# Kernel optimization log

Measured on AMD Instinct MI355X. Metric: run time of the kernel, lower is better.

The kernel has to match this reference:

```python
import jax, jax.numpy as jnp
import numpy as np

N_QUBITS, Q_DEPTH, N_OUTPUT, BATCH = 8, 6, 8, 16384
_C = np.complex64
_H = (np.array([[1, 1], [1, -1]]) / np.sqrt(2)).astype(_C)
_PX = np.array([[0, 1], [1, 0]], dtype=_C)
_PY = np.array([[0, -1j], [1j, 0]], dtype=_C)
_PZ = np.array([[1, 0], [0, -1]], dtype=_C)

def _swap_rows(n, i, j):
    m = np.eye(n, dtype=_C)
    m[[i, j]] = m[[j, i]]
    return m

_CNOT = _swap_rows(4, 2, 3)          # flip target when control=1
_CZ = np.diag(np.array([1, 1, 1, -1], dtype=_C))
_CSWAP = _swap_rows(8, 5, 6)         # swap |101> <-> |110>
_TOF = _swap_rows(8, 6, 7)           # swap |110> <-> |111>


def _apply(state, U, wires):
    """Apply k-qubit gate U (2^k x 2^k, shared across batch) on given wires.
    state: [B] + [2]*N_QUBITS complex tensor."""
    k = len(wires)
    axes = [w + 1 for w in wires]
    st = jnp.moveaxis(state, axes, list(range(1, k + 1)))
    shp = st.shape
    st = jnp.einsum('ij,bjr->bir', jnp.asarray(U, st.dtype), st.reshape(shp[0], 2 ** k, -1))
    return jnp.moveaxis(st.reshape(shp), list(range(1, k + 1)), axes)


def _apply_batched(state, U, wire):
    """Apply per-sample single-qubit gate U [B,2,2] on `wire`."""
    st = jnp.moveaxis(state, wire + 1, 1)
    shp = st.shape
    st = jnp.einsum('bij,bjr->bir', U, st.reshape(shp[0], 2, -1))
    return jnp.moveaxis(st.reshape(shp), 1, wire + 1)


def _rot_mat(axis, theta):
    """Scalar-angle RX/RY/RZ (axis 0/1/2), PennyLane convention exp(-i theta P / 2)."""
    c = jnp.cos(theta / 2)
    s = jnp.sin(theta / 2)
    z = jnp.zeros_like(c)
    if axis == 0:    # RX
        re = jnp.stack([jnp.stack([c, z]), jnp.stack([z, c])])
        im = jnp.stack([jnp.stack([z, -s]), jnp.stack([-s, z])])
    elif axis == 1:  # RY
        re = jnp.stack([jnp.stack([c, -s]), jnp.stack([s, c])])
        im = jnp.zeros((2, 2), dtype=c.dtype)
    else:            # RZ
        re = jnp.stack([jnp.stack([c, z]), jnp.stack([z, c])])
        im = jnp.stack([jnp.stack([-s, z]), jnp.stack([z, s])])
    return (re.astype(jnp.complex64) + 1j * im.astype(jnp.complex64))


def _ry_batched(theta):
    """Per-sample RY matrices: theta [B] -> [B,2,2] complex64."""
    c = jnp.cos(theta / 2)
    s = jnp.sin(theta / 2)
    U = jnp.stack([jnp.stack([c, -s], -1), jnp.stack([s, c], -1)], -2)
    return U.astype(jnp.complex64)


def _forward(input_features, q_params, d_ry, d_rot, d_g2):
    B = input_features.shape[0]
    n = N_QUBITS
    qw = q_params.reshape(Q_DEPTH, n)
    # |0...0> state, shape [B] + [2]*n
    basis = jnp.zeros((2 ** n,), jnp.complex64).at[0].set(1.0)
    state = (jnp.ones((B, 1), jnp.complex64) * basis[None, :]).reshape((B,) + (2,) * n)
    for w in range(n):
        state = _apply(state, _H, [w])
    two_q = {5: _CNOT, 8: _CZ}
    three_q = {6: _CSWAP, 7: _TOF}
    one_q = {1: _H, 2: _PX, 3: _PY, 4: _PZ}
    for layer in range(Q_DEPTH):
        for node in range(n):
            li, ni = layer % 6, node % 4
            if d_ry[li, ni]:
                state = _apply_batched(state, _ry_batched(input_features[:, node]), node)
            rot = int(d_rot[li, ni])
            if rot < 3:
                state = _apply(state, _rot_mat(rot, qw[layer, node]), [node])
            g2 = int(d_g2[li, ni])
            if g2 in one_q:
                state = _apply(state, one_q[g2], [node])
            elif g2 in two_q:
                state = _apply(state, two_q[g2], [node, (node + 1) % n])
            elif g2 in three_q:
                state = _apply(state, three_q[g2], [node, (node + 1) % n, (node + 2) % n])
    probs = state.real ** 2 + state.imag ** 2  # [B] + [2]*n
    exps = []
    for p in range(N_OUTPUT):
        axes = tuple(i for i in range(1, n + 1) if i != p + 1)
        m = probs.sum(axis=axes)  # [B, 2]
        exps.append(m[:, 0] - m[:, 1])
    return jnp.stack(exps, axis=1)  # [B, N_OUTPUT] float32


def setup_inputs() -> dict:
    key = jax.random.key(0)
    k1, k2, k3, k4, k5 = jax.random.split(key, 5)
    return {
        'input_features': jax.random.normal(k1, (BATCH, N_QUBITS), jnp.float32),
        'q_params': jax.random.normal(k2, (Q_DEPTH * N_QUBITS,), jnp.float32),
        'design_ry': jax.random.randint(k3, (6, 4), 0, 2, jnp.int32),
        'design_rot': jax.random.randint(k4, (6, 4), 0, 4, jnp.int32),
        'design_gate2': jax.random.randint(k5, (6, 4), 0, 9, jnp.int32),
    }


def reference(input_features, q_params, design_ry, design_rot, design_gate2):
    # The circuit design is a static (architecture) choice -> host constants.
    d_ry = np.asarray(design_ry)
    d_rot = np.asarray(design_rot)
    d_g2 = np.asarray(design_gate2)
    return _forward(input_features, q_params, d_ry, d_rot, d_g2)
```

## Files before the change

kernel.cpp:

```cpp
#include <hip/hip_runtime.h>
#include <stdint.h>

#define NQ 8

#define HALF_INV2PI 0.07957747154594767f

typedef float f32x2 __attribute__((ext_vector_type(2)));

__device__ __forceinline__ f32x2 pk2(float x, float y) { f32x2 r; r.x = x; r.y = y; return r; }
__device__ __forceinline__ f32x2 pkb(float x)          { f32x2 r; r.x = x; r.y = x; return r; }

__device__ __forceinline__ f32x2 pk_fma(f32x2 a, f32x2 b, f32x2 c) {
    f32x2 d;
    asm("v_pk_fma_f32 %0, %1, %2, %3" : "=v"(d) : "v"(a), "v"(b), "v"(c));
    return d;
}
__device__ __forceinline__ f32x2 pk_mul(f32x2 a, f32x2 b) {
    f32x2 d;
    asm("v_pk_mul_f32 %0, %1, %2" : "=v"(d) : "v"(a), "v"(b));
    return d;
}
__device__ __forceinline__ f32x2 pk_fma_sa_nh(f32x2 a, f32x2 b, f32x2 c) {
    f32x2 d;
    asm("v_pk_fma_f32 %0, %1, %2, %3 op_sel:[1,0,0] op_sel_hi:[0,1,1] neg_hi:[0,1,0]"
        : "=v"(d) : "v"(a), "v"(b), "v"(c));
    return d;
}
__device__ __forceinline__ f32x2 pk_fma_sa_nl(f32x2 a, f32x2 b, f32x2 c) {
    f32x2 d;
    asm("v_pk_fma_f32 %0, %1, %2, %3 op_sel:[1,0,0] op_sel_hi:[0,1,1] neg_lo:[0,1,0]"
        : "=v"(d) : "v"(a), "v"(b), "v"(c));
    return d;
}
__device__ __forceinline__ f32x2 pk_fma_nh(f32x2 a, f32x2 b, f32x2 c) {
    f32x2 d;
    asm("v_pk_fma_f32 %0, %1, %2, %3 neg_hi:[0,1,0]"
        : "=v"(d) : "v"(a), "v"(b), "v"(c));
    return d;
}

template<int XM>
__device__ __forceinline__ float sx(float v) {
    if constexpr (XM == 0) return v;
    const int x = __float_as_int(v);
    int r;
    if constexpr (XM == 1)      r = __builtin_amdgcn_update_dpp(0, x, 0xB1,  0xF, 0xF, true);
    else if constexpr (XM == 2) r = __builtin_amdgcn_update_dpp(0, x, 0x4E,  0xF, 0xF, true);
    else if constexpr (XM == 8) r = __builtin_amdgcn_update_dpp(0, x, 0x128, 0xF, 0xF, true);
    else                        r = __builtin_amdgcn_ds_swizzle(x, (XM << 10) | 0x1F);
    return __int_as_float(r);
}

template<int XM>
__device__ __forceinline__ f32x2 sxp(f32x2 v) {
    f32x2 r; r.x = sx<XM>(v.x); r.y = sx<XM>(v.y); return r;
}
template<int XM>
__device__ __forceinline__ f32x2 sxp_swap(f32x2 v) {
    f32x2 r; r.x = sx<XM>(v.y); r.y = sx<XM>(v.x); return r;
}

__device__ __forceinline__ void swapv(f32x2& a, f32x2& b) { f32x2 t = a; a = b; b = t; }

__device__ __forceinline__ float rfl(float x) {
    return __int_as_float(__builtin_amdgcn_readfirstlane(__float_as_int(x)));
}


template<int Q>
__device__ __forceinline__ void realGate(f32x2 (&v)[8], int laneq,
                                         float a, float b, float d, float e)
{
    if constexpr (Q < 3) {
        constexpr int M = 1 << Q;
        const f32x2 a2 = pkb(a), b2 = pkb(b), d2 = pkb(d), e2 = pkb(e);
#pragma unroll
        for (int i = 0; i < 8; i++) if (!(i & M)) {
            const int j = i | M;
            const f32x2 x0 = v[i], x1 = v[j];
            v[i] = pk_fma(a2, x0, pk_mul(b2, x1));
            v[j] = pk_fma(d2, x0, pk_mul(e2, x1));
        }
    } else {
        constexpr int XM = 1 << (Q - 3);
        const int bit = (laneq >> (Q - 3)) & 1;
        const f32x2 sc2 = pkb(bit ? e : a);
        const f32x2 pc2 = pkb(bit ? d : b);
#pragma unroll
        for (int i = 0; i < 8; i++) {
            const f32x2 p = sxp<XM>(v[i]);
            v[i] = pk_fma(sc2, v[i], pk_mul(pc2, p));
        }
    }
}

template<int Q>
__device__ __forceinline__ void applyRX(f32x2 (&v)[8], int laneq, float c, float s)
{
    const f32x2 cc = pkb(c), ss = pkb(s);
    if constexpr (Q < 3) {
        constexpr int M = 1 << Q;
#pragma unroll
        for (int i = 0; i < 8; i++) if (!(i & M)) {
            const int j = i | M;
            const f32x2 x0 = v[i], x1 = v[j];
            v[i] = pk_fma_sa_nh(x1, ss, pk_mul(cc, x0));
            v[j] = pk_fma_sa_nh(x0, ss, pk_mul(cc, x1));
        }
    } else {
        constexpr int XM = 1 << (Q - 3);
#pragma unroll
        for (int i = 0; i < 8; i++) {
            const f32x2 ps = sxp_swap<XM>(v[i]);
            v[i] = pk_fma_nh(ps, ss, pk_mul(cc, v[i]));
        }
    }
}

template<int Q>
__device__ __forceinline__ void applyRZ(f32x2 (&v)[8], int laneq, float c, float s)
{
    const f32x2 cc = pkb(c);
    if constexpr (Q >= 3) {
        const int bit = (laneq >> (Q - 3)) & 1;
        const float t = bit ? -s : s;
        const f32x2 tt = pkb(t);
#pragma unroll
        for (int i = 0; i < 8; i++)
            v[i] = pk_fma_sa_nh(v[i], tt, pk_mul(cc, v[i]));
    } else {
        const f32x2 ss = pkb(s);
#pragma unroll
        for (int i = 0; i < 8; i++) {
            if ((i >> Q) & 1) v[i] = pk_fma_sa_nl(v[i], ss, pk_mul(cc, v[i]));
            else              v[i] = pk_fma_sa_nh(v[i], ss, pk_mul(cc, v[i]));
        }
    }
}

template<int Q>
__device__ __forceinline__ void applyZ(f32x2 (&v)[8], int laneq)
{
    if constexpr (Q >= 3) {
        const bool f = ((laneq >> (Q - 3)) & 1) != 0;
#pragma unroll
        for (int i = 0; i < 8; i++) {
            v[i].x = f ? -v[i].x : v[i].x;
            v[i].y = f ? -v[i].y : v[i].y;
        }
    } else {
#pragma unroll
        for (int i = 0; i < 8; i++) if ((i >> Q) & 1) {
            v[i].x = -v[i].x; v[i].y = -v[i].y;
        }
    }
}

template<int Q>
__device__ __forceinline__ void applyX(f32x2 (&v)[8], int laneq)
{
    if constexpr (Q < 3) {
        constexpr int M = 1 << Q;
#pragma unroll
        for (int i = 0; i < 8; i++) if (!(i & M)) {
            swapv(v[i], v[i | M]);
        }
    } else {
        constexpr int XM = 1 << (Q - 3);
#pragma unroll
        for (int i = 0; i < 8; i++) {
            v[i] = sxp<XM>(v[i]);
        }
    }
}

template<int Q>
__device__ __forceinline__ void applyY(f32x2 (&v)[8], int laneq)
{
    if constexpr (Q < 3) {
        constexpr int M = 1 << Q;
#pragma unroll
        for (int i = 0; i < 8; i++) if (!(i & M)) {
            const int j = i | M;
            const f32x2 x0 = v[i], x1 = v[j];
            v[i] = pk2(x1.y, -x1.x);
            v[j] = pk2(-x0.y, x0.x);
        }
    } else {
        constexpr int XM = 1 << (Q - 3);
        const int bit = (laneq >> (Q - 3)) & 1;
#pragma unroll
        for (int i = 0; i < 8; i++) {
            const f32x2 p = sxp<XM>(v[i]);
            v[i].x = bit ? -p.y : p.y;
            v[i].y = bit ? p.x : -p.x;
        }
    }
}

template<int C, int T>
__device__ __forceinline__ void applyCZ(f32x2 (&v)[8], int laneq)
{
#pragma unroll
    for (int i = 0; i < 8; i++) {
        const int g = i | (laneq << 3);
        const bool f = (((g >> C) & (g >> T)) & 1) != 0;
        v[i].x = f ? -v[i].x : v[i].x;
        v[i].y = f ? -v[i].y : v[i].y;
    }
}

template<int CM, int M>
__device__ __forceinline__ void applyCPerm(f32x2 (&v)[8], int laneq)
{
    constexpr int LX  = M >> 3;
    constexpr int PL  = M & 7;
    constexpr int CML = CM & 7;
    constexpr int CMH = CM >> 3;
    if constexpr (LX != 0) {
#pragma unroll
        for (int i = 0; i < 8; i++) {
            if ((i & CML) == CML) {
                const f32x2 p = sxp<LX>(v[i]);
                if constexpr (CMH != 0) {
                    const bool c = (laneq & CMH) == CMH;
                    v[i].x = c ? p.x : v[i].x;
                    v[i].y = c ? p.y : v[i].y;
                } else {
                    v[i] = p;
                }
            }
        }
    } else {
#pragma unroll
        for (int i = 0; i < 8; i++) {
            if (!(i & PL) && ((i & CML) == CML)) {
                const int j = i | PL;
                if constexpr (CMH != 0) {
                    const bool c = (laneq & CMH) == CMH;
                    const f32x2 t0 = v[i];
                    v[i].x = c ? v[j].x : v[i].x;  v[i].y = c ? v[j].y : v[i].y;
                    v[j].x = c ? t0.x : v[j].x;    v[j].y = c ? t0.y : v[j].y;
                } else {
                    swapv(v[i], v[j]);
                }
            }
        }
    }
}

template<int C, int T1, int T2>
__device__ __forceinline__ void applyCSWAP(f32x2 (&v)[8], int laneq)
{
    constexpr int M  = (1 << T1) | (1 << T2);
    constexpr int LX = M >> 3;
    constexpr int PL = M & 7;

    if constexpr (LX == 0) {
#pragma unroll
        for (int i = 0; i < 8; i++) {
            if (((i >> T1) & 1) && !((i >> T2) & 1)) {
                bool skip = false;
                if constexpr (C < 3) { if (!((i >> C) & 1)) skip = true; }
                if (!skip) {
                    const int j = i ^ PL;
                    if constexpr (C >= 3) {
                        const bool c = ((laneq >> (C - 3)) & 1) != 0;
                        const f32x2 t0 = v[i];
                        v[i].x = c ? v[j].x : v[i].x;  v[i].y = c ? v[j].y : v[i].y;
                        v[j].x = c ? t0.x : v[j].x;    v[j].y = c ? t0.y : v[j].y;
                    } else {
                        swapv(v[i], v[j]);
                    }
                }
            }
        }
    } else if constexpr (PL == 0) {
        bool c = ((((laneq >> (T1 - 3)) ^ (laneq >> (T2 - 3))) & 1) != 0);
        if constexpr (C >= 3) c = c && (((laneq >> (C - 3)) & 1) != 0);
#pragma unroll
        for (int i = 0; i < 8; i++) {
            bool skip = false;
            if constexpr (C < 3) { if (!((i >> C) & 1)) skip = true; }
            if (!skip) {
                const f32x2 p = sxp<LX>(v[i]);
                v[i].x = c ? p.x : v[i].x;
                v[i].y = c ? p.y : v[i].y;
            }
        }
    } else {
        constexpr int TL = (PL == (1 << T1)) ? T2 : T1;
        const bool laneT = ((laneq >> (TL - 3)) & 1) != 0;
        bool cc = true;
        if constexpr (C >= 3) cc = ((laneq >> (C - 3)) & 1) != 0;
#pragma unroll
        for (int i = 0; i < 8; i++) {
            if (!(i & PL)) {
                bool skip = false;
                if constexpr (C < 3) { if (!((i >> C) & 1)) skip = true; }
                if (!skip) {
                    const int j = i | PL;
                    const f32x2 a = sxp<LX>(v[j]);
                    const f32x2 b = sxp<LX>(v[i]);
                    const bool ci = cc && laneT;
                    const bool cj = cc && !laneT;
                    v[i].x = ci ? a.x : v[i].x;  v[i].y = ci ? a.y : v[i].y;
                    v[j].x = cj ? b.x : v[j].x;  v[j].y = cj ? b.y : v[j].y;
                }
            }
        }
    }
}

template<int N>
__device__ __forceinline__ void nodeStep(f32x2 (&v)[8], int laneq,
                                         const float2* ryCS,
                                         const float (&rotC)[8], const float (&rotS)[8],
                                         int dryL, int drotL, int dg2L)
{
    constexpr int N1 = (N + 1) & 7;
    constexpr int N2 = (N + 2) & 7;
    constexpr int SL = N & 3;

    const bool ryOn = ((dryL >> SL) & 1) != 0;
    const int rot = (drotL >> (2 * SL)) & 3;

    if (rot < 3) {
        const float cb = rotC[N], sb = rotS[N];
        if (ryOn && rot == 1) {
            const float2 a = ryCS[N];
            const float c = cb * a.x - sb * a.y;
            const float s = sb * a.x + cb * a.y;
            realGate<N>(v, laneq, c, -s, s, c);
        } else {
            if (ryOn) {
                const float2 a = ryCS[N];
                realGate<N>(v, laneq, a.x, -a.y, a.y, a.x);
            }
            if (rot == 0)      applyRX<N>(v, laneq, cb, sb);
            else if (rot == 1) realGate<N>(v, laneq, cb, -sb, sb, cb);
            else               applyRZ<N>(v, laneq, cb, sb);
        }
    } else if (ryOn) {
        const float2 a = ryCS[N];
        realGate<N>(v, laneq, a.x, -a.y, a.y, a.x);
    }

    const int g2 = (dg2L >> (4 * SL)) & 15;
    switch (g2) {
        case 1: {
            const float r = 0.70710678118654752f;
            realGate<N>(v, laneq, r, r, r, -r);
        } break;
        case 2: applyX<N>(v, laneq); break;
        case 3: applyY<N>(v, laneq); break;
        case 4: applyZ<N>(v, laneq); break;
        case 5: applyCPerm<(1 << N), (1 << N1)>(v, laneq); break;
        case 6: applyCSWAP<N, N1, N2>(v, laneq); break;
        case 7: applyCPerm<(1 << N) | (1 << N1), (1 << N2)>(v, laneq); break;
        case 8: applyCZ<N, N1>(v, laneq); break;
        default: break;
    }
}

__global__ __launch_bounds__(256, 4) void qsim_kernel(
    const float* __restrict__ feats,
    const float* __restrict__ qp,
    const int* __restrict__ dry,
    const int* __restrict__ drot,
    const int* __restrict__ dg2,
    float* __restrict__ out,
    int B)
{
    __shared__ float2 lds_ry[8][8];
    __shared__ float2 lds_rot[48];

    const int tid   = threadIdx.x;
    const int laneq = tid & 31;
    const int grp   = tid >> 5;
    const int b     = blockIdx.x * 8 + grp;

    if (tid < 48) {
        const float th = qp[tid] * HALF_INV2PI;
        lds_rot[tid] = make_float2(__builtin_amdgcn_cosf(th), __builtin_amdgcn_sinf(th));
    }
    if (laneq < 8) {
        const float th = feats[(size_t)b * NQ + laneq] * HALF_INV2PI;
        lds_ry[grp][laneq] = make_float2(__builtin_amdgcn_cosf(th), __builtin_amdgcn_sinf(th));
    }

    uint32_t dryP = 0;
    uint64_t drotP = 0;
    uint32_t g2P0 = 0, g2P1 = 0, g2P2 = 0;
#pragma unroll
    for (int q = 0; q < 6; q++) {
        const int4 a = ((const int4*)dry)[q];
        dryP |= (uint32_t)(__builtin_amdgcn_readfirstlane(a.x) & 1) << (4 * q + 0);
        dryP |= (uint32_t)(__builtin_amdgcn_readfirstlane(a.y) & 1) << (4 * q + 1);
        dryP |= (uint32_t)(__builtin_amdgcn_readfirstlane(a.z) & 1) << (4 * q + 2);
        dryP |= (uint32_t)(__builtin_amdgcn_readfirstlane(a.w) & 1) << (4 * q + 3);
        const int4 r = ((const int4*)drot)[q];
        drotP |= (uint64_t)(__builtin_amdgcn_readfirstlane(r.x) & 3) << (8 * q + 0);
        drotP |= (uint64_t)(__builtin_amdgcn_readfirstlane(r.y) & 3) << (8 * q + 2);
        drotP |= (uint64_t)(__builtin_amdgcn_readfirstlane(r.z) & 3) << (8 * q + 4);
        drotP |= (uint64_t)(__builtin_amdgcn_readfirstlane(r.w) & 3) << (8 * q + 6);
        const int4 g = ((const int4*)dg2)[q];
        const uint32_t gg = ((uint32_t)(__builtin_amdgcn_readfirstlane(g.x) & 15))
                          | ((uint32_t)(__builtin_amdgcn_readfirstlane(g.y) & 15) << 4)
                          | ((uint32_t)(__builtin_amdgcn_readfirstlane(g.z) & 15) << 8)
                          | ((uint32_t)(__builtin_amdgcn_readfirstlane(g.w) & 15) << 12);
        if      (q == 0) g2P0 |= gg;
        else if (q == 1) g2P0 |= gg << 16;
        else if (q == 2) g2P1 |= gg;
        else if (q == 3) g2P1 |= gg << 16;
        else if (q == 4) g2P2 |= gg;
        else             g2P2 |= gg << 16;
    }

    __syncthreads();

    const float2* ryCS  = &lds_ry[grp][0];

    f32x2 v[8];
#pragma unroll
    for (int i = 0; i < 8; i++) { v[i] = pk2(0.0625f, 0.0f); }

#pragma unroll 1
    for (int layer = 0; layer < 6; layer++) {
        const int dryL  = (int)((dryP >> (layer * 4)) & 0xF);
        const int drotL = (int)((drotP >> (layer * 8)) & 0xFF);
        const uint32_t g2w = (layer >= 4) ? g2P2 : ((layer >= 2) ? g2P1 : g2P0);
        const int dg2L  = (int)((g2w >> ((layer & 1) * 16)) & 0xFFFF);

        float rotC[8], rotS[8];
#pragma unroll
        for (int n = 0; n < 8; n++) {
            const float2 t = lds_rot[layer * NQ + n];
            rotC[n] = rfl(t.x);
            rotS[n] = rfl(t.y);
        }

        nodeStep<0>(v, laneq, ryCS, rotC, rotS, dryL, drotL, dg2L);
        nodeStep<1>(v, laneq, ryCS, rotC, rotS, dryL, drotL, dg2L);
        nodeStep<2>(v, laneq, ryCS, rotC, rotS, dryL, drotL, dg2L);
        nodeStep<3>(v, laneq, ryCS, rotC, rotS, dryL, drotL, dg2L);
        nodeStep<4>(v, laneq, ryCS, rotC, rotS, dryL, drotL, dg2L);
        nodeStep<5>(v, laneq, ryCS, rotC, rotS, dryL, drotL, dg2L);
        nodeStep<6>(v, laneq, ryCS, rotC, rotS, dryL, drotL, dg2L);
        nodeStep<7>(v, laneq, ryCS, rotC, rotS, dryL, drotL, dg2L);
    }

    float tot = 0.f, s0 = 0.f, s1 = 0.f, s2 = 0.f;
#pragma unroll
    for (int i = 0; i < 8; i++) {
        const float p = v[i].x * v[i].x + v[i].y * v[i].y;
        tot += p;
        if (!(i & 1)) s0 += p;
        if (!(i & 2)) s1 += p;
        if (!(i & 4)) s2 += p;
    }
    float e[3] = { 2.f * s0 - tot, 2.f * s1 - tot, 2.f * s2 - tot };

#pragma unroll
    for (int q = 0; q < 3; q++) {
        e[q] += sx<1>(e[q]);
        e[q] += sx<2>(e[q]);
        e[q] += sx<4>(e[q]);
        e[q] += sx<8>(e[q]);
        e[q] += sx<16>(e[q]);
    }
    { float pv = sx<1>(tot);  tot = (laneq & 1)  ? (pv - tot) : (pv + tot); }
    { float pv = sx<2>(tot);  tot = (laneq & 2)  ? (pv - tot) : (pv + tot); }
    { float pv = sx<4>(tot);  tot = (laneq & 4)  ? (pv - tot) : (pv + tot); }
    { float pv = sx<8>(tot);  tot = (laneq & 8)  ? (pv - tot) : (pv + tot); }
    { float pv = sx<16>(tot); tot = (laneq & 16) ? (pv - tot) : (pv + tot); }

    float* ob = out + (size_t)b * NQ;
    if (laneq == 0) { ob[0] = e[0]; ob[1] = e[1]; ob[2] = e[2]; }
    if (laneq && !(laneq & (laneq - 1)))
        ob[3 + __builtin_ctz(laneq)] = tot;
}

extern "C" void kernel_launch(void* const* d_in, const int* in_sizes, int n_in,
                              void* d_out, int out_size, void* d_ws, size_t ws_size,
                              hipStream_t stream)
{
    (void)n_in; (void)out_size; (void)d_ws; (void)ws_size;
    const float* feats   = (const float*)d_in[0];
    const float* qparams = (const float*)d_in[1];
    const int* dry       = (const int*)d_in[2];
    const int* drot      = (const int*)d_in[3];
    const int* dg2       = (const int*)d_in[4];
    float* out           = (float*)d_out;

    const int B = in_sizes[0] / NQ;
    const int blocks = (B + 7) / 8;
    qsim_kernel<<<blocks, 256, 0, stream>>>(feats, qparams, dry, drot, dg2, out, B);
}
```

Before: 108.9 us.

## Remap qubit lanes so cross-lane shuffles use DPP and permlane32 swaps

Changes the mapping of threads to amplitudes within a wave: lane bit 2 now selects the sample and the upper qubit bits move up one position, so each logical XOR-shuffle becomes a physical permutation. Shuffles on lane masks 1, 2, 3 and 8 use DPP, and the top qubit bit uses permlane32_swap instead of ds_swizzle. The aim is to replace LDS-path swizzles with cheaper DPP and permlane operations in the gate kernels. The trade-off is a more intricate lane mapping and an extra XOR per cross-half exchange.

```diff
diff --git a/kernel.cpp b/kernel.cpp
--- a/kernel.cpp
+++ b/kernel.cpp
@@ -6,6 +6,7 @@
 #define HALF_INV2PI 0.07957747154594767f
 
 typedef float f32x2 __attribute__((ext_vector_type(2)));
+typedef unsigned int u32x2 __attribute__((ext_vector_type(2)));
 
 __device__ __forceinline__ f32x2 pk2(float x, float y) { f32x2 r; r.x = x; r.y = y; return r; }
 __device__ __forceinline__ f32x2 pkb(float x)          { f32x2 r; r.x = x; r.y = x; return r; }
@@ -40,24 +41,31 @@
 }
 
 template<int XM>
-__device__ __forceinline__ float sx(float v) {
+__device__ __forceinline__ float sx(float v, int laneq) {
     if constexpr (XM == 0) return v;
-    const int x = __float_as_int(v);
-    int r;
-    if constexpr (XM == 1)      r = __builtin_amdgcn_update_dpp(0, x, 0xB1,  0xF, 0xF, true);
-    else if constexpr (XM == 2) r = __builtin_amdgcn_update_dpp(0, x, 0x4E,  0xF, 0xF, true);
-    else if constexpr (XM == 8) r = __builtin_amdgcn_update_dpp(0, x, 0x128, 0xF, 0xF, true);
-    else                        r = __builtin_amdgcn_ds_swizzle(x, (XM << 10) | 0x1F);
-    return __int_as_float(r);
+    constexpr int PH  = (XM & 3) | ((XM & 28) << 1);
+    constexpr int PLO = PH & 31;
+    int x = __float_as_int(v);
+    if constexpr (PLO == 1)      x = __builtin_amdgcn_update_dpp(0, x, 0xB1,  0xF, 0xF, true);
+    else if constexpr (PLO == 2) x = __builtin_amdgcn_update_dpp(0, x, 0x4E,  0xF, 0xF, true);
+    else if constexpr (PLO == 3) x = __builtin_amdgcn_update_dpp(0, x, 0x1B,  0xF, 0xF, true);
+    else if constexpr (PLO == 8) x = __builtin_amdgcn_update_dpp(0, x, 0x128, 0xF, 0xF, true);
+    else if constexpr (PLO != 0) x = __builtin_amdgcn_ds_swizzle(x, (PLO << 10) | 0x1F);
+    if constexpr ((PH & 32) != 0) {
+        const u32x2 t = __builtin_amdgcn_permlane32_swap((unsigned)x, (unsigned)x, false, false);
+        x = (int)(t[0] ^ t[1]) ^ x;
+    }
+    (void)laneq;
+    return __int_as_float(x);
 }
 
 template<int XM>
-__device__ __forceinline__ f32x2 sxp(f32x2 v) {
-    f32x2 r; r.x = sx<XM>(v.x); r.y = sx<XM>(v.y); return r;
+__device__ __forceinline__ f32x2 sxp(f32x2 v, int laneq) {
+    f32x2 r; r.x = sx<XM>(v.x, laneq); r.y = sx<XM>(v.y, laneq); return r;
 }
 template<int XM>
-__device__ __forceinline__ f32x2 sxp_swap(f32x2 v) {
-    f32x2 r; r.x = sx<XM>(v.y); r.y = sx<XM>(v.x); return r;
+__device__ __forceinline__ f32x2 sxp_swap(f32x2 v, int laneq) {
+    f32x2 r; r.x = sx<XM>(v.y, laneq); r.y = sx<XM>(v.x, laneq); return r;
 }
 
 __device__ __forceinline__ void swapv(f32x2& a, f32x2& b) { f32x2 t = a; a = b; b = t; }
@@ -88,7 +96,7 @@
         const f32x2 pc2 = pkb(bit ? d : b);
 #pragma unroll
         for (int i = 0; i < 8; i++) {
-            const f32x2 p = sxp<XM>(v[i]);
+            const f32x2 p = sxp<XM>(v[i], laneq);
             v[i] = pk_fma(sc2, v[i], pk_mul(pc2, p));
         }
     }
@@ -111,7 +119,7 @@
         constexpr int XM = 1 << (Q - 3);
 #pragma unroll
         for (int i = 0; i < 8; i++) {
-            const f32x2 ps = sxp_swap<XM>(v[i]);
+            const f32x2 ps = sxp_swap<XM>(v[i], laneq);
             v[i] = pk_fma_nh(ps, ss, pk_mul(cc, v[i]));
         }
     }
@@ -169,7 +177,7 @@
         constexpr int XM = 1 << (Q - 3);
 #pragma unroll
         for (int i = 0; i < 8; i++) {
-            v[i] = sxp<XM>(v[i]);
+            v[i] = sxp<XM>(v[i], laneq);
         }
     }
 }
@@ -191,7 +199,7 @@
         const int bit = (laneq >> (Q - 3)) & 1;
 #pragma unroll
         for (int i = 0; i < 8; i++) {
-            const f32x2 p = sxp<XM>(v[i]);
+            const f32x2 p = sxp<XM>(v[i], laneq);
             v[i].x = bit ? -p.y : p.y;
             v[i].y = bit ? p.x : -p.x;
         }
@@ -221,7 +229,7 @@
 #pragma unroll
         for (int i = 0; i < 8; i++) {
             if ((i & CML) == CML) {
-                const f32x2 p = sxp<LX>(v[i]);
+                const f32x2 p = sxp<LX>(v[i], laneq);
                 if constexpr (CMH != 0) {
                     const bool c = (laneq & CMH) == CMH;
                     v[i].x = c ? p.x : v[i].x;
@@ -283,7 +291,7 @@
             bool skip = false;
             if constexpr (C < 3) { if (!((i >> C) & 1)) skip = true; }
             if (!skip) {
-                const f32x2 p = sxp<LX>(v[i]);
+                const f32x2 p = sxp<LX>(v[i], laneq);
                 v[i].x = c ? p.x : v[i].x;
                 v[i].y = c ? p.y : v[i].y;
             }
@@ -300,8 +308,8 @@
                 if constexpr (C < 3) { if (!((i >> C) & 1)) skip = true; }
                 if (!skip) {
                     const int j = i | PL;
-                    const f32x2 a = sxp<LX>(v[j]);
-                    const f32x2 b = sxp<LX>(v[i]);
+                    const f32x2 a = sxp<LX>(v[j], laneq);
+                    const f32x2 b = sxp<LX>(v[i], laneq);
                     const bool ci = cc && laneT;
                     const bool cj = cc && !laneT;
                     v[i].x = ci ? a.x : v[i].x;  v[i].y = ci ? a.y : v[i].y;
@@ -376,8 +384,10 @@
     __shared__ float2 lds_rot[48];
 
     const int tid   = threadIdx.x;
-    const int laneq = tid & 31;
-    const int grp   = tid >> 5;
+    const int p     = tid & 63;
+    const int laneq = (p & 3) | ((p >> 1) & 28);
+    const int e     = (p >> 2) & 1;
+    const int grp   = (tid >> 6) * 2 + e;
     const int b     = blockIdx.x * 8 + grp;
 
     if (tid < 48) {
@@ -453,30 +463,30 @@
     float tot = 0.f, s0 = 0.f, s1 = 0.f, s2 = 0.f;
 #pragma unroll
     for (int i = 0; i < 8; i++) {
-        const float p = v[i].x * v[i].x + v[i].y * v[i].y;
-        tot += p;
-        if (!(i & 1)) s0 += p;
-        if (!(i & 2)) s1 += p;
-        if (!(i & 4)) s2 += p;
-    }
-    float e[3] = { 2.f * s0 - tot, 2.f * s1 - tot, 2.f * s2 - tot };
+        const float pw = v[i].x * v[i].x + v[i].y * v[i].y;
+        tot += pw;
+        if (!(i & 1)) s0 += pw;
+        if (!(i & 2)) s1 += pw;
+        if (!(i & 4)) s2 += pw;
+    }
+    float ez[3] = { 2.f * s0 - tot, 2.f * s1 - tot, 2.f * s2 - tot };
 
 #pragma unroll
     for (int q = 0; q < 3; q++) {
-        e[q] += sx<1>(e[q]);
-        e[q] += sx<2>(e[q]);
-        e[q] += sx<4>(e[q]);
-        e[q] += sx<8>(e[q]);
-        e[q] += sx<16>(e[q]);
-    }
-    { float pv = sx<1>(tot);  tot = (laneq & 1)  ? (pv - tot) : (pv + tot); }
-    { float pv = sx<2>(tot);  tot = (laneq & 2)  ? (pv - tot) : (pv + tot); }
-    { float pv = sx<4>(tot);  tot = (laneq & 4)  ? (pv - tot) : (pv + tot); }
-    { float pv = sx<8>(tot);  tot = (laneq & 8)  ? (pv - tot) : (pv + tot); }
-    { float pv = sx<16>(tot); tot = (laneq & 16) ? (pv - tot) : (pv + tot); }
+        ez[q] += sx<1>(ez[q], laneq);
+        ez[q] += sx<2>(ez[q], laneq);
+        ez[q] += sx<4>(ez[q], laneq);
+        ez[q] += sx<8>(ez[q], laneq);
+        ez[q] += sx<16>(ez[q], laneq);
+    }
+    { float pv = sx<1>(tot, laneq);  tot = (laneq & 1)  ? (pv - tot) : (pv + tot); }
+    { float pv = sx<2>(tot, laneq);  tot = (laneq & 2)  ? (pv - tot) : (pv + tot); }
+    { float pv = sx<4>(tot, laneq);  tot = (laneq & 4)  ? (pv - tot) : (pv + tot); }
+    { float pv = sx<8>(tot, laneq);  tot = (laneq & 8)  ? (pv - tot) : (pv + tot); }
+    { float pv = sx<16>(tot, laneq); tot = (laneq & 16) ? (pv - tot) : (pv + tot); }
 
     float* ob = out + (size_t)b * NQ;
-    if (laneq == 0) { ob[0] = e[0]; ob[1] = e[1]; ob[2] = e[2]; }
+    if (laneq == 0) { ob[0] = ez[0]; ob[1] = ez[1]; ob[2] = ez[2]; }
     if (laneq && !(laneq & (laneq - 1)))
         ob[3 + __builtin_ctz(laneq)] = tot;
 }
```

Result: slower. 118.5 us (+8.8%).
